# Kernel optimization log

Measured on AMD Instinct MI355X. Metric: run time of the kernel, lower is better.

The kernel has to match this reference:

```python
import jax, jax.numpy as jnp
import numpy as np

N = 100000        # nodes
E = 1600000       # edges
F_IN = 32         # raw node features
C = 128           # out_channels / hidden
L = 5             # gated graph conv layers
G = 1024          # number of graphs in batch


def setup_inputs() -> dict:
    key = jax.random.key(0)
    ks = jax.random.split(key, 12)
    x = jax.random.normal(ks[0], (N, F_IN), dtype=jnp.float32)
    edge_index = jax.random.randint(ks[1], (2, E), 0, N, dtype=jnp.int32)
    edge_weight = jax.random.uniform(ks[2], (E,), dtype=jnp.float32)
    batch = jnp.sort(jax.random.randint(ks[3], (N,), 0, G, dtype=jnp.int32))
    # parameters (scaled small, fan-in style)
    W_emb = jax.random.normal(ks[4], (F_IN, C), dtype=jnp.float32) / np.sqrt(F_IN)
    b_emb = jnp.zeros((C,), dtype=jnp.float32)
    W = jax.random.normal(ks[5], (L, C, C), dtype=jnp.float32) / np.sqrt(C)
    W_ih = jax.random.normal(ks[6], (3 * C, C), dtype=jnp.float32) / np.sqrt(C)
    W_hh = jax.random.normal(ks[7], (3 * C, C), dtype=jnp.float32) / np.sqrt(C)
    b_ih = jnp.zeros((3 * C,), dtype=jnp.float32)
    b_hh = jnp.zeros((3 * C,), dtype=jnp.float32)
    W_prop = jax.random.normal(ks[8], (C, 1), dtype=jnp.float32) / np.sqrt(C)
    b_prop = jnp.zeros((1,), dtype=jnp.float32)
    return {"x": x, "edge_index": edge_index, "edge_weight": edge_weight,
            "batch": batch, "W_emb": W_emb, "b_emb": b_emb, "W": W,
            "W_ih": W_ih, "W_hh": W_hh, "b_ih": b_ih, "b_hh": b_hh,
            "W_prop": W_prop, "b_prop": b_prop}


def _gated_graph_conv(h, src, dst, edge_weight, W, W_ih, W_hh, b_ih, b_hh):
    n_nodes = h.shape[0]

    def step(h, Wl):
        m = h @ Wl                                    # [N,C] per-layer linear
        msg = m[src] * edge_weight[:, None]           # gather + edge weight [E,C]
        agg = jax.ops.segment_sum(msg, dst, num_segments=n_nodes)  # scatter-add
        # torch GRUCell (gate order r, z, n)
        gi = agg @ W_ih.T + b_ih                      # [N,3C]
        gh = h @ W_hh.T + b_hh
        i_r, i_z, i_n = jnp.split(gi, 3, axis=-1)
        h_r, h_z, h_n = jnp.split(gh, 3, axis=-1)
        r = jax.nn.sigmoid(i_r + h_r)
        z = jax.nn.sigmoid(i_z + h_z)
        n = jnp.tanh(i_n + r * h_n)
        h_new = (1.0 - z) * n + z * h
        return h_new, None

    h, _ = jax.lax.scan(step, h, W)
    return h


def reference(x, edge_index, edge_weight, batch, W_emb, b_emb, W,
              W_ih, W_hh, b_ih, b_hh, W_prop, b_prop):
    h0 = x @ W_emb + b_emb                            # node embedding [N,C]
    src, dst = edge_index[0], edge_index[1]
    h = _gated_graph_conv(h0, src, dst, edge_weight, W, W_ih, W_hh, b_ih, b_hh)
    node_prop = h @ W_prop + b_prop                   # [N,1]
    graph_prop = jax.ops.segment_sum(node_prop, batch, num_segments=G)  # [G,1]
    return graph_prop.squeeze(1)                      # [G]
```

## Files before the change

### kernel.cpp

```cpp
#include <hip/hip_runtime.h>

#define NN 100000
#define CC 128
#define EE 1600000
#define GG 1024
#define LL 5

typedef __attribute__((ext_vector_type(8))) short bf16x8;
typedef __attribute__((ext_vector_type(4))) float f32x4;

__device__ __forceinline__ float sigmoidf_(float x) { return 1.0f / (1.0f + __expf(-x)); }
__device__ __forceinline__ float tanhf_(float x) {
  float xx = fminf(15.0f, fmaxf(-15.0f, x));
  float t = __expf(-2.0f * xx);
  return (1.0f - t) / (1.0f + t);
}
__device__ __forceinline__ unsigned short f2bf(float x) {
  unsigned int u = __float_as_uint(x);
  return (unsigned short)((u + 0x7fffu + ((u >> 16) & 1u)) >> 16);
}
__device__ __forceinline__ float bflo(unsigned int u) { return __uint_as_float(u << 16); }
__device__ __forceinline__ float bfhi(unsigned int u) { return __uint_as_float(u & 0xffff0000u); }
__device__ __forceinline__ float bf2f(unsigned short v) { return __uint_as_float((unsigned)v << 16); }

#define PK_WHH 192
#define PK_FUSE (192 * LL)
#define PK_DEG ((NN + 256 + 255) / 256)
#define PK_TOTAL (PK_WHH + PK_FUSE + PK_DEG + 1)

__global__ __launch_bounds__(256) void pack_all_kernel(
    const float* __restrict__ W, const float* __restrict__ W_ih,
    const float* __restrict__ W_hh,
    unsigned short* __restrict__ Whh_p, unsigned short* __restrict__ Wfuse_p,
    int* __restrict__ deg, float* __restrict__ out)
{
  const int b = blockIdx.x;
  const int tid = threadIdx.x;
  if (b < PK_WHH) {
    int t = b * 256 + tid;
    int i = t & 7, l = (t >> 3) & 63, q = t >> 9;
    int ks = q & 3, cb = q >> 2;
    int k = ks * 32 + 8 * (l >> 4) + i;
    int c = cb * 16 + (l & 15);
    Whh_p[t] = f2bf(W_hh[(size_t)c * CC + k]);
  } else if (b < PK_WHH + PK_FUSE) {
    int idx = b - PK_WHH;
    int layer = idx / 192;
    int t = (idx % 192) * 256 + tid;
    int i = t & 7, l = (t >> 3) & 63, q = t >> 9;
    int ks = q & 3, cb = q >> 2;
    int k = ks * 32 + 8 * (l >> 4) + i;
    int c = cb * 16 + (l & 15);
    const float* wl = W + (size_t)layer * CC * CC + (size_t)k * CC;
    const float* wi = W_ih + (size_t)c * CC;
    float acc = 0.f;
    #pragma unroll 8
    for (int j = 0; j < CC; ++j) acc = fmaf(wl[j], wi[j], acc);
    Wfuse_p[(size_t)layer * 49152 + t] = f2bf(acc);
  } else if (b < PK_WHH + PK_FUSE + PK_DEG) {
    int i = (b - PK_WHH - PK_FUSE) * 256 + tid;
    if (i < NN + 256) deg[i] = 0;
  } else {
    #pragma unroll
    for (int i = 0; i < 4; ++i) out[i * 256 + tid] = 0.0f;
  }
}


__global__ __launch_bounds__(256) void hist_kernel(const int* __restrict__ eidx,
                                                   int* __restrict__ deg)
{
  int e = blockIdx.x * blockDim.x + threadIdx.x;
  if (e < EE) atomicAdd(&deg[eidx[EE + e]], 1);
}

__global__ __launch_bounds__(256) void scan1_kernel(const int* __restrict__ deg,
                                                    int* __restrict__ bsum)
{
  __shared__ int red[4];
  int base = blockIdx.x * 1024 + threadIdx.x * 4;
  int s = 0;
  #pragma unroll
  for (int i = 0; i < 4; ++i) { int idx = base + i; if (idx < NN) s += deg[idx]; }
  #pragma unroll
  for (int off = 32; off; off >>= 1) s += __shfl_down(s, off, 64);
  if ((threadIdx.x & 63) == 0) red[threadIdx.x >> 6] = s;
  __syncthreads();
  if (threadIdx.x == 0) bsum[blockIdx.x] = red[0] + red[1] + red[2] + red[3];
}

__global__ __launch_bounds__(64) void scan2_kernel(int* __restrict__ bsum, int nb)
{
  const int lane = threadIdx.x;
  int carry = 0;
  for (int base = 0; base < nb; base += 64) {
    int i = base + lane;
    int v = (i < nb) ? bsum[i] : 0;
    const int orig = v;
    #pragma unroll
    for (int off = 1; off < 64; off <<= 1) {
      int u = __shfl_up(v, off, 64);
      if (lane >= off) v += u;
    }
    if (i < nb) bsum[i] = v - orig + carry;
    carry += __shfl(v, 63, 64);
  }
}

__global__ __launch_bounds__(256) void scan3_kernel(const int* __restrict__ deg,
                                                    const int* __restrict__ bsum,
                                                    int* __restrict__ row_ptr,
                                                    int* __restrict__ cursor)
{
  __shared__ int ts[256];
  const int tid = threadIdx.x;
  const int base = blockIdx.x * 1024 + tid * 4;
  int v[4]; int s = 0;
  #pragma unroll
  for (int i = 0; i < 4; ++i) { int idx = base + i; v[i] = (idx < NN) ? deg[idx] : 0; s += v[i]; }
  ts[tid] = s; __syncthreads();
  for (int off = 1; off < 256; off <<= 1) {
    int t = (tid >= off) ? ts[tid - off] : 0;
    __syncthreads();
    ts[tid] += t;
    __syncthreads();
  }
  int excl = bsum[blockIdx.x] + ts[tid] - s;
  #pragma unroll
  for (int i = 0; i < 4; ++i) {
    int idx = base + i;
    if (idx < NN) { row_ptr[idx] = excl; cursor[idx] = excl; excl += v[i]; }
  }
  if (blockIdx.x == 0 && tid == 0) row_ptr[NN] = EE;
}

__global__ __launch_bounds__(256) void fill_kernel(const int* __restrict__ eidx,
                                                   const float* __restrict__ ew,
                                                   int* __restrict__ cursor,
                                                   int2* __restrict__ csr_sw)
{
  int e = blockIdx.x * blockDim.x + threadIdx.x;
  if (e < EE) {
    int d = eidx[EE + e];
    int p = atomicAdd(&cursor[d], 1);
    csr_sw[p] = make_int2(eidx[e], __float_as_int(ew[e]));
  }
}


__global__ __launch_bounds__(128) void embed_kernel(
    const float* __restrict__ x, const float* __restrict__ W_emb,
    const float* __restrict__ b_emb, unsigned short* __restrict__ h_bf)
{
  const int node = blockIdx.x;
  const int c = threadIdx.x;
  float acc = b_emb[c];
  #pragma unroll
  for (int k = 0; k < 32; ++k)
    acc = fmaf(x[node * 32 + k], W_emb[k * CC + c], acc);
  h_bf[(size_t)node * CC + c] = f2bf(acc);
}

__global__ __launch_bounds__(256) void aggregate_kernel(
    const unsigned short* __restrict__ h_bf, const int* __restrict__ row_ptr,
    const int2* __restrict__ csr_sw, unsigned short* __restrict__ agg_bf)
{
  const int lane = threadIdx.x & 63;
  const int node = (blockIdx.x * blockDim.x + threadIdx.x) >> 6;
  if (node >= NN) return;
  const int q = lane >> 4;
  const int t = lane & 15;
  const int beg = row_ptr[node], end = row_ptr[node + 1];

  float acc[8] = {0.f, 0.f, 0.f, 0.f, 0.f, 0.f, 0.f, 0.f};
  const int last = end - 1;

  for (int j = beg; j < end; j += 16) {
    const int e0 = j + q, e1 = j + 4 + q, e2 = j + 8 + q, e3 = j + 12 + q;
    const int i0 = min(e0, last), i1 = min(e1, last);
    const int i2 = min(e2, last), i3 = min(e3, last);
    const int2 r0 = csr_sw[i0], r1 = csr_sw[i1], r2 = csr_sw[i2], r3 = csr_sw[i3];
    const float w0 = (e0 < end) ? __int_as_float(r0.y) : 0.0f;
    const float w1 = (e1 < end) ? __int_as_float(r1.y) : 0.0f;
    const float w2 = (e2 < end) ? __int_as_float(r2.y) : 0.0f;
    const float w3 = (e3 < end) ? __int_as_float(r3.y) : 0.0f;
    const uint4 u0 = *(const uint4*)(h_bf + (size_t)r0.x * CC + t * 8);
    const uint4 u1 = *(const uint4*)(h_bf + (size_t)r1.x * CC + t * 8);
    const uint4 u2 = *(const uint4*)(h_bf + (size_t)r2.x * CC + t * 8);
    const uint4 u3 = *(const uint4*)(h_bf + (size_t)r3.x * CC + t * 8);
    acc[0] = fmaf(bflo(u0.x), w0, acc[0]); acc[1] = fmaf(bfhi(u0.x), w0, acc[1]);
    acc[2] = fmaf(bflo(u0.y), w0, acc[2]); acc[3] = fmaf(bfhi(u0.y), w0, acc[3]);
    acc[4] = fmaf(bflo(u0.z), w0, acc[4]); acc[5] = fmaf(bfhi(u0.z), w0, acc[5]);
    acc[6] = fmaf(bflo(u0.w), w0, acc[6]); acc[7] = fmaf(bfhi(u0.w), w0, acc[7]);
    acc[0] = fmaf(bflo(u1.x), w1, acc[0]); acc[1] = fmaf(bfhi(u1.x), w1, acc[1]);
    acc[2] = fmaf(bflo(u1.y), w1, acc[2]); acc[3] = fmaf(bfhi(u1.y), w1, acc[3]);
    acc[4] = fmaf(bflo(u1.z), w1, acc[4]); acc[5] = fmaf(bfhi(u1.z), w1, acc[5]);
    acc[6] = fmaf(bflo(u1.w), w1, acc[6]); acc[7] = fmaf(bfhi(u1.w), w1, acc[7]);
    acc[0] = fmaf(bflo(u2.x), w2, acc[0]); acc[1] = fmaf(bfhi(u2.x), w2, acc[1]);
    acc[2] = fmaf(bflo(u2.y), w2, acc[2]); acc[3] = fmaf(bfhi(u2.y), w2, acc[3]);
    acc[4] = fmaf(bflo(u2.z), w2, acc[4]); acc[5] = fmaf(bfhi(u2.z), w2, acc[5]);
    acc[6] = fmaf(bflo(u2.w), w2, acc[6]); acc[7] = fmaf(bfhi(u2.w), w2, acc[7]);
    acc[0] = fmaf(bflo(u3.x), w3, acc[0]); acc[1] = fmaf(bfhi(u3.x), w3, acc[1]);
    acc[2] = fmaf(bflo(u3.y), w3, acc[2]); acc[3] = fmaf(bfhi(u3.y), w3, acc[3]);
    acc[4] = fmaf(bflo(u3.z), w3, acc[4]); acc[5] = fmaf(bfhi(u3.z), w3, acc[5]);
    acc[6] = fmaf(bflo(u3.w), w3, acc[6]); acc[7] = fmaf(bfhi(u3.w), w3, acc[7]);
  }

  #pragma unroll
  for (int i = 0; i < 8; ++i) {
    acc[i] += __shfl_xor(acc[i], 16, 64);
    acc[i] += __shfl_xor(acc[i], 32, 64);
  }

  if (q == 0) {
    uint4 o;
    o.x = (unsigned)f2bf(acc[0]) | ((unsigned)f2bf(acc[1]) << 16);
    o.y = (unsigned)f2bf(acc[2]) | ((unsigned)f2bf(acc[3]) << 16);
    o.z = (unsigned)f2bf(acc[4]) | ((unsigned)f2bf(acc[5]) << 16);
    o.w = (unsigned)f2bf(acc[6]) | ((unsigned)f2bf(acc[7]) << 16);
    *(uint4*)(agg_bf + (size_t)node * CC + t * 8) = o;
  }
}

__global__ __launch_bounds__(256) void gru_kernel(
    const unsigned short* __restrict__ agg_bf, unsigned short* __restrict__ h_bf,
    const unsigned short* __restrict__ Wfuse_p, const unsigned short* __restrict__ Whh_p,
    const float* __restrict__ b_ih, const float* __restrict__ b_hh)
{
  __shared__ unsigned short hbuf[4][32][136];
  const int lane = threadIdx.x & 63;
  const int wave = threadIdx.x >> 6;
  const int node0 = blockIdx.x * 128 + wave * 32;
  if (node0 >= NN) return;
  const int col16 = lane & 15, grp = lane >> 4;

  #pragma unroll
  for (int i = 0; i < 8; ++i) {
    const int chunk = lane + 64 * i;
    const int row = chunk >> 4, c16 = chunk & 15;
    uint4 v = *(const uint4*)(h_bf + (size_t)(node0 + row) * CC + c16 * 8);
    *(uint4*)&hbuf[wave][row][c16 * 8] = v;
  }

  bf16x8 aA[2][4], aH[2][4];
  #pragma unroll
  for (int t = 0; t < 2; ++t) {
    const unsigned short* arow = agg_bf + (size_t)(node0 + t * 16 + col16) * CC + grp * 8;
    #pragma unroll
    for (int ks = 0; ks < 4; ++ks) {
      aA[t][ks] = *(const bf16x8*)(arow + ks * 32);
      aH[t][ks] = *(const bf16x8*)&hbuf[wave][t * 16 + col16][grp * 8 + ks * 32];
    }
  }

  const f32x4 z4 = {0.f, 0.f, 0.f, 0.f};

  #pragma unroll
  for (int cb = 0; cb < 8; ++cb) {
    f32x4 air[2] = {z4, z4}, ahr[2] = {z4, z4};
    f32x4 aiz[2] = {z4, z4}, ahz[2] = {z4, z4};
    f32x4 ain[2] = {z4, z4}, ahn[2] = {z4, z4};
    #pragma unroll
    for (int ks = 0; ks < 4; ++ks) {
      const size_t or_ = (size_t)((cb * 4 + ks) * 64 + lane) * 8;
      const size_t oz_ = (size_t)(((8 + cb) * 4 + ks) * 64 + lane) * 8;
      const size_t on_ = (size_t)(((16 + cb) * 4 + ks) * 64 + lane) * 8;
      bf16x8 bir = *(const bf16x8*)(Wfuse_p + or_);
      bf16x8 bhr = *(const bf16x8*)(Whh_p + or_);
      bf16x8 biz = *(const bf16x8*)(Wfuse_p + oz_);
      bf16x8 bhz = *(const bf16x8*)(Whh_p + oz_);
      bf16x8 bin = *(const bf16x8*)(Wfuse_p + on_);
      bf16x8 bhn = *(const bf16x8*)(Whh_p + on_);
      #pragma unroll
      for (int t = 0; t < 2; ++t) {
        air[t] = __builtin_amdgcn_mfma_f32_16x16x32_bf16(aA[t][ks], bir, air[t], 0, 0, 0);
        ahr[t] = __builtin_amdgcn_mfma_f32_16x16x32_bf16(aH[t][ks], bhr, ahr[t], 0, 0, 0);
        aiz[t] = __builtin_amdgcn_mfma_f32_16x16x32_bf16(aA[t][ks], biz, aiz[t], 0, 0, 0);
        ahz[t] = __builtin_amdgcn_mfma_f32_16x16x32_bf16(aH[t][ks], bhz, ahz[t], 0, 0, 0);
        ain[t] = __builtin_amdgcn_mfma_f32_16x16x32_bf16(aA[t][ks], bin, ain[t], 0, 0, 0);
        ahn[t] = __builtin_amdgcn_mfma_f32_16x16x32_bf16(aH[t][ks], bhn, ahn[t], 0, 0, 0);
      }
    }
    const int o = cb * 16 + col16;
    const float bir_ = b_ih[o],       bhr_ = b_hh[o];
    const float biz_ = b_ih[128 + o], bhz_ = b_hh[128 + o];
    const float bin_ = b_ih[256 + o], bhn_ = b_hh[256 + o];
    #pragma unroll
    for (int t = 0; t < 2; ++t) {
      #pragma unroll
      for (int r = 0; r < 4; ++r) {
        float rr = sigmoidf_(air[t][r] + ahr[t][r] + bir_ + bhr_);
        float zz = sigmoidf_(aiz[t][r] + ahz[t][r] + biz_ + bhz_);
        float nn = tanhf_(ain[t][r] + bin_ + rr * (ahn[t][r] + bhn_));
        const int row = t * 16 + grp * 4 + r;
        float ho = bf2f(hbuf[wave][row][o]);
        h_bf[(size_t)(node0 + row) * CC + o] = f2bf((1.0f - zz) * nn + zz * ho);
      }
    }
  }
}

__global__ __launch_bounds__(256) void prop_kernel(
    const unsigned short* __restrict__ h_bf, const int* __restrict__ batch,
    const float* __restrict__ Wp, const float* __restrict__ bp,
    float* __restrict__ out)
{
  const int lane = threadIdx.x & 63;
  const int wid = (blockIdx.x * blockDim.x + threadIdx.x) >> 6;
  const int nw = (gridDim.x * blockDim.x) >> 6;
  for (int node = wid; node < NN; node += nw) {
    unsigned int u = *(const unsigned int*)(h_bf + (size_t)node * CC + 2 * lane);
    float v = bflo(u) * Wp[2 * lane] + bfhi(u) * Wp[2 * lane + 1];
    #pragma unroll
    for (int off = 32; off > 0; off >>= 1) v += __shfl_down(v, off, 64);
    if (lane == 0) atomicAdd(&out[batch[node]], v + bp[0]);
  }
}

extern "C" void kernel_launch(void* const* d_in, const int* in_sizes, int n_in,
                              void* d_out, int out_size, void* d_ws, size_t ws_size,
                              hipStream_t stream)
{
  const float* x      = (const float*)d_in[0];
  const int*   eidx   = (const int*)d_in[1];
  const float* ew     = (const float*)d_in[2];
  const int*   batch  = (const int*)d_in[3];
  const float* W_emb  = (const float*)d_in[4];
  const float* b_emb  = (const float*)d_in[5];
  const float* W      = (const float*)d_in[6];
  const float* W_ih   = (const float*)d_in[7];
  const float* W_hh   = (const float*)d_in[8];
  const float* b_ih   = (const float*)d_in[9];
  const float* b_hh   = (const float*)d_in[10];
  const float* W_prop = (const float*)d_in[11];
  const float* b_prop = (const float*)d_in[12];
  float* out = (float*)d_out;

  char* p = (char*)d_ws;
  unsigned short* h_bf  = (unsigned short*)p; p += (size_t)NN * CC * sizeof(short);
  unsigned short* agg   = (unsigned short*)p; p += (size_t)NN * CC * sizeof(short);
  int2* csr_sw          = (int2*)p;           p += (size_t)EE * sizeof(int2);
  unsigned short* Wfuse_p = (unsigned short*)p; p += (size_t)LL * 49152 * sizeof(short);
  unsigned short* Whh_p = (unsigned short*)p; p += (size_t)49152 * sizeof(short);
  int* deg     = (int*)p;                     p += (size_t)(NN + 256) * sizeof(int);
  int* row_ptr = (int*)p;                     p += (size_t)(NN + 256) * sizeof(int);
  int* cursor  = (int*)p;                     p += (size_t)(NN + 256) * sizeof(int);
  int* bsum    = (int*)p;                     p += 1024 * sizeof(int);

  const int NB_SCAN = (NN + 1023) / 1024;
  const int EB = (EE + 255) / 256;
  const int MB2 = (NN + 127) / 128;

  pack_all_kernel<<<PK_TOTAL, 256, 0, stream>>>(W, W_ih, W_hh, Whh_p, Wfuse_p, deg, out);

  hist_kernel<<<EB, 256, 0, stream>>>(eidx, deg);
  scan1_kernel<<<NB_SCAN, 256, 0, stream>>>(deg, bsum);
  scan2_kernel<<<1, 64, 0, stream>>>(bsum, NB_SCAN);
  scan3_kernel<<<NB_SCAN, 256, 0, stream>>>(deg, bsum, row_ptr, cursor);
  fill_kernel<<<EB, 256, 0, stream>>>(eidx, ew, cursor, csr_sw);

  embed_kernel<<<NN, 128, 0, stream>>>(x, W_emb, b_emb, h_bf);

  for (int l = 0; l < LL; ++l) {
    aggregate_kernel<<<(NN + 3) / 4, 256, 0, stream>>>(h_bf, row_ptr, csr_sw, agg);
    gru_kernel<<<MB2, 256, 0, stream>>>(agg, h_bf,
                                        Wfuse_p + (size_t)l * 49152, Whh_p, b_ih, b_hh);
  }

  prop_kernel<<<2048, 256, 0, stream>>>(h_bf, batch, W_prop, b_prop, out);
}
```

Before: 881.4 us.

## Switch GRU matmuls to 32x32x16 MFMA and deepen aggregate edge unroll

The GRU kernel moves from 16x16x32 bf16 MFMA tiles (two row tiles, eight column blocks) to 32x32x16 MFMA tiles (one 32-row tile, four column blocks), and the packed weight layouts are changed to match. This is meant to halve the number of B-fragment weight loads per wave and use the larger MFMA shape. Separately, the aggregate kernel processes 32 edges per iteration instead of 16, issuing all index and feature loads before the FMAs so more gathers are in flight. The costs are higher register pressure from the 16-wide accumulators and the extra in-flight loads, and a non-unrolled outer loop in the GRU kernel.

```diff
diff --git a/kernel.cpp b/kernel.cpp
--- a/kernel.cpp
+++ b/kernel.cpp
@@ -7,7 +7,7 @@
 #define LL 5
 
 typedef __attribute__((ext_vector_type(8))) short bf16x8;
-typedef __attribute__((ext_vector_type(4))) float f32x4;
+typedef __attribute__((ext_vector_type(16))) float f32x16;
 
 __device__ __forceinline__ float sigmoidf_(float x) { return 1.0f / (1.0f + __expf(-x)); }
 __device__ __forceinline__ float tanhf_(float x) {
@@ -39,20 +39,20 @@
   if (b < PK_WHH) {
     int t = b * 256 + tid;
     int i = t & 7, l = (t >> 3) & 63, q = t >> 9;
-    int ks = q & 3, cb = q >> 2;
-    int k = ks * 32 + 8 * (l >> 4) + i;
-    int c = cb * 16 + (l & 15);
-    Whh_p[t] = f2bf(W_hh[(size_t)c * CC + k]);
+    int ks = q & 7, cb = q >> 3;
+    int k = ks * 16 + 8 * (l >> 5) + i;
+    int o = cb * 32 + (l & 31);
+    Whh_p[t] = f2bf(W_hh[(size_t)o * CC + k]);
   } else if (b < PK_WHH + PK_FUSE) {
     int idx = b - PK_WHH;
     int layer = idx / 192;
     int t = (idx % 192) * 256 + tid;
     int i = t & 7, l = (t >> 3) & 63, q = t >> 9;
-    int ks = q & 3, cb = q >> 2;
-    int k = ks * 32 + 8 * (l >> 4) + i;
-    int c = cb * 16 + (l & 15);
+    int ks = q & 7, cb = q >> 3;
+    int k = ks * 16 + 8 * (l >> 5) + i;
+    int o = cb * 32 + (l & 31);
     const float* wl = W + (size_t)layer * CC * CC + (size_t)k * CC;
-    const float* wi = W_ih + (size_t)c * CC;
+    const float* wi = W_ih + (size_t)o * CC;
     float acc = 0.f;
     #pragma unroll 8
     for (int j = 0; j < CC; ++j) acc = fmaf(wl[j], wi[j], acc);
@@ -175,19 +175,30 @@
   float acc[8] = {0.f, 0.f, 0.f, 0.f, 0.f, 0.f, 0.f, 0.f};
   const int last = end - 1;
 
-  for (int j = beg; j < end; j += 16) {
-    const int e0 = j + q, e1 = j + 4 + q, e2 = j + 8 + q, e3 = j + 12 + q;
-    const int i0 = min(e0, last), i1 = min(e1, last);
-    const int i2 = min(e2, last), i3 = min(e3, last);
-    const int2 r0 = csr_sw[i0], r1 = csr_sw[i1], r2 = csr_sw[i2], r3 = csr_sw[i3];
+  for (int j = beg; j < end; j += 32) {
+    const int e0 = j + q,      e1 = j + 4 + q,  e2 = j + 8 + q,  e3 = j + 12 + q;
+    const int e4 = j + 16 + q, e5 = j + 20 + q, e6 = j + 24 + q, e7 = j + 28 + q;
+    const int2 r0 = csr_sw[min(e0, last)], r1 = csr_sw[min(e1, last)];
+    const int2 r2 = csr_sw[min(e2, last)], r3 = csr_sw[min(e3, last)];
+    const int2 r4 = csr_sw[min(e4, last)], r5 = csr_sw[min(e5, last)];
+    const int2 r6 = csr_sw[min(e6, last)], r7 = csr_sw[min(e7, last)];
+    const uint4 u0 = *(const uint4*)(h_bf + (size_t)r0.x * CC + t * 8);
+    const uint4 u1 = *(const uint4*)(h_bf + (size_t)r1.x * CC + t * 8);
+    const uint4 u2 = *(const uint4*)(h_bf + (size_t)r2.x * CC + t * 8);
+    const uint4 u3 = *(const uint4*)(h_bf + (size_t)r3.x * CC + t * 8);
+    const uint4 u4 = *(const uint4*)(h_bf + (size_t)r4.x * CC + t * 8);
+    const uint4 u5 = *(const uint4*)(h_bf + (size_t)r5.x * CC + t * 8);
+    const uint4 u6 = *(const uint4*)(h_bf + (size_t)r6.x * CC + t * 8);
+    const uint4 u7 = *(const uint4*)(h_bf + (size_t)r7.x * CC + t * 8);
     const float w0 = (e0 < end) ? __int_as_float(r0.y) : 0.0f;
     const float w1 = (e1 < end) ? __int_as_float(r1.y) : 0.0f;
     const float w2 = (e2 < end) ? __int_as_float(r2.y) : 0.0f;
     const float w3 = (e3 < end) ? __int_as_float(r3.y) : 0.0f;
-    const uint4 u0 = *(const uint4*)(h_bf + (size_t)r0.x * CC + t * 8);
-    const uint4 u1 = *(const uint4*)(h_bf + (size_t)r1.x * CC + t * 8);
-    const uint4 u2 = *(const uint4*)(h_bf + (size_t)r2.x * CC + t * 8);
-    const uint4 u3 = *(const uint4*)(h_bf + (size_t)r3.x * CC + t * 8);
+    const float w4 = (e4 < end) ? __int_as_float(r4.y) : 0.0f;
+    const float w5 = (e5 < end) ? __int_as_float(r5.y) : 0.0f;
+    const float w6 = (e6 < end) ? __int_as_float(r6.y) : 0.0f;
+    const float w7 = (e7 < end) ? __int_as_float(r7.y) : 0.0f;
+
     acc[0] = fmaf(bflo(u0.x), w0, acc[0]); acc[1] = fmaf(bfhi(u0.x), w0, acc[1]);
     acc[2] = fmaf(bflo(u0.y), w0, acc[2]); acc[3] = fmaf(bfhi(u0.y), w0, acc[3]);
     acc[4] = fmaf(bflo(u0.z), w0, acc[4]); acc[5] = fmaf(bfhi(u0.z), w0, acc[5]);
@@ -204,6 +215,22 @@
     acc[2] = fmaf(bflo(u3.y), w3, acc[2]); acc[3] = fmaf(bfhi(u3.y), w3, acc[3]);
     acc[4] = fmaf(bflo(u3.z), w3, acc[4]); acc[5] = fmaf(bfhi(u3.z), w3, acc[5]);
     acc[6] = fmaf(bflo(u3.w), w3, acc[6]); acc[7] = fmaf(bfhi(u3.w), w3, acc[7]);
+    acc[0] = fmaf(bflo(u4.x), w4, acc[0]); acc[1] = fmaf(bfhi(u4.x), w4, acc[1]);
+    acc[2] = fmaf(bflo(u4.y), w4, acc[2]); acc[3] = fmaf(bfhi(u4.y), w4, acc[3]);
+    acc[4] = fmaf(bflo(u4.z), w4, acc[4]); acc[5] = fmaf(bfhi(u4.z), w4, acc[5]);
+    acc[6] = fmaf(bflo(u4.w), w4, acc[6]); acc[7] = fmaf(bfhi(u4.w), w4, acc[7]);
+    acc[0] = fmaf(bflo(u5.x), w5, acc[0]); acc[1] = fmaf(bfhi(u5.x), w5, acc[1]);
+    acc[2] = fmaf(bflo(u5.y), w5, acc[2]); acc[3] = fmaf(bfhi(u5.y), w5, acc[3]);
+    acc[4] = fmaf(bflo(u5.z), w5, acc[4]); acc[5] = fmaf(bfhi(u5.z), w5, acc[5]);
+    acc[6] = fmaf(bflo(u5.w), w5, acc[6]); acc[7] = fmaf(bfhi(u5.w), w5, acc[7]);
+    acc[0] = fmaf(bflo(u6.x), w6, acc[0]); acc[1] = fmaf(bfhi(u6.x), w6, acc[1]);
+    acc[2] = fmaf(bflo(u6.y), w6, acc[2]); acc[3] = fmaf(bfhi(u6.y), w6, acc[3]);
+    acc[4] = fmaf(bflo(u6.z), w6, acc[4]); acc[5] = fmaf(bfhi(u6.z), w6, acc[5]);
+    acc[6] = fmaf(bflo(u6.w), w6, acc[6]); acc[7] = fmaf(bfhi(u6.w), w6, acc[7]);
+    acc[0] = fmaf(bflo(u7.x), w7, acc[0]); acc[1] = fmaf(bfhi(u7.x), w7, acc[1]);
+    acc[2] = fmaf(bflo(u7.y), w7, acc[2]); acc[3] = fmaf(bfhi(u7.y), w7, acc[3]);
+    acc[4] = fmaf(bflo(u7.z), w7, acc[4]); acc[5] = fmaf(bfhi(u7.z), w7, acc[5]);
+    acc[6] = fmaf(bflo(u7.w), w7, acc[6]); acc[7] = fmaf(bfhi(u7.w), w7, acc[7]);
   }
 
   #pragma unroll
@@ -232,7 +259,8 @@
   const int wave = threadIdx.x >> 6;
   const int node0 = blockIdx.x * 128 + wave * 32;
   if (node0 >= NN) return;
-  const int col16 = lane & 15, grp = lane >> 4;
+  const int l31 = lane & 31;
+  const int kg = lane >> 5;
 
   #pragma unroll
   for (int i = 0; i < 8; ++i) {
@@ -242,60 +270,50 @@
     *(uint4*)&hbuf[wave][row][c16 * 8] = v;
   }
 
-  bf16x8 aA[2][4], aH[2][4];
-  #pragma unroll
-  for (int t = 0; t < 2; ++t) {
-    const unsigned short* arow = agg_bf + (size_t)(node0 + t * 16 + col16) * CC + grp * 8;
-    #pragma unroll
-    for (int ks = 0; ks < 4; ++ks) {
-      aA[t][ks] = *(const bf16x8*)(arow + ks * 32);
-      aH[t][ks] = *(const bf16x8*)&hbuf[wave][t * 16 + col16][grp * 8 + ks * 32];
+  bf16x8 aA[8], aH[8];
+  {
+    const unsigned short* arow = agg_bf + (size_t)(node0 + l31) * CC + kg * 8;
+    #pragma unroll
+    for (int ks = 0; ks < 8; ++ks) {
+      aA[ks] = *(const bf16x8*)(arow + ks * 16);
+      aH[ks] = *(const bf16x8*)&hbuf[wave][l31][ks * 16 + kg * 8];
     }
   }
 
-  const f32x4 z4 = {0.f, 0.f, 0.f, 0.f};
-
-  #pragma unroll
-  for (int cb = 0; cb < 8; ++cb) {
-    f32x4 air[2] = {z4, z4}, ahr[2] = {z4, z4};
-    f32x4 aiz[2] = {z4, z4}, ahz[2] = {z4, z4};
-    f32x4 ain[2] = {z4, z4}, ahn[2] = {z4, z4};
-    #pragma unroll
-    for (int ks = 0; ks < 4; ++ks) {
-      const size_t or_ = (size_t)((cb * 4 + ks) * 64 + lane) * 8;
-      const size_t oz_ = (size_t)(((8 + cb) * 4 + ks) * 64 + lane) * 8;
-      const size_t on_ = (size_t)(((16 + cb) * 4 + ks) * 64 + lane) * 8;
-      bf16x8 bir = *(const bf16x8*)(Wfuse_p + or_);
-      bf16x8 bhr = *(const bf16x8*)(Whh_p + or_);
-      bf16x8 biz = *(const bf16x8*)(Wfuse_p + oz_);
-      bf16x8 bhz = *(const bf16x8*)(Whh_p + oz_);
-      bf16x8 bin = *(const bf16x8*)(Wfuse_p + on_);
-      bf16x8 bhn = *(const bf16x8*)(Whh_p + on_);
-      #pragma unroll
-      for (int t = 0; t < 2; ++t) {
-        air[t] = __builtin_amdgcn_mfma_f32_16x16x32_bf16(aA[t][ks], bir, air[t], 0, 0, 0);
-        ahr[t] = __builtin_amdgcn_mfma_f32_16x16x32_bf16(aH[t][ks], bhr, ahr[t], 0, 0, 0);
-        aiz[t] = __builtin_amdgcn_mfma_f32_16x16x32_bf16(aA[t][ks], biz, aiz[t], 0, 0, 0);
-        ahz[t] = __builtin_amdgcn_mfma_f32_16x16x32_bf16(aH[t][ks], bhz, ahz[t], 0, 0, 0);
-        ain[t] = __builtin_amdgcn_mfma_f32_16x16x32_bf16(aA[t][ks], bin, ain[t], 0, 0, 0);
-        ahn[t] = __builtin_amdgcn_mfma_f32_16x16x32_bf16(aH[t][ks], bhn, ahn[t], 0, 0, 0);
-      }
+  const f32x16 z16 = {0.f};
+
+  for (int cc = 0; cc < 4; ++cc) {
+    f32x16 air = z16, ahr = z16, aiz = z16, ahz = z16, ain = z16, ahn = z16;
+    #pragma unroll
+    for (int ks = 0; ks < 8; ++ks) {
+      const size_t fr = (size_t)(((cc     ) * 8 + ks) * 64 + lane) * 8;
+      const size_t fz = (size_t)(((4 + cc) * 8 + ks) * 64 + lane) * 8;
+      const size_t fn = (size_t)(((8 + cc) * 8 + ks) * 64 + lane) * 8;
+      bf16x8 bir = *(const bf16x8*)(Wfuse_p + fr);
+      bf16x8 bhr = *(const bf16x8*)(Whh_p + fr);
+      bf16x8 biz = *(const bf16x8*)(Wfuse_p + fz);
+      bf16x8 bhz = *(const bf16x8*)(Whh_p + fz);
+      bf16x8 bin = *(const bf16x8*)(Wfuse_p + fn);
+      bf16x8 bhn = *(const bf16x8*)(Whh_p + fn);
+      air = __builtin_amdgcn_mfma_f32_32x32x16_bf16(aA[ks], bir, air, 0, 0, 0);
+      ahr = __builtin_amdgcn_mfma_f32_32x32x16_bf16(aH[ks], bhr, ahr, 0, 0, 0);
+      aiz = __builtin_amdgcn_mfma_f32_32x32x16_bf16(aA[ks], biz, aiz, 0, 0, 0);
+      ahz = __builtin_amdgcn_mfma_f32_32x32x16_bf16(aH[ks], bhz, ahz, 0, 0, 0);
+      ain = __builtin_amdgcn_mfma_f32_32x32x16_bf16(aA[ks], bin, ain, 0, 0, 0);
+      ahn = __builtin_amdgcn_mfma_f32_32x32x16_bf16(aH[ks], bhn, ahn, 0, 0, 0);
     }
-    const int o = cb * 16 + col16;
+    const int o = cc * 32 + l31;
     const float bir_ = b_ih[o],       bhr_ = b_hh[o];
     const float biz_ = b_ih[128 + o], bhz_ = b_hh[128 + o];
     const float bin_ = b_ih[256 + o], bhn_ = b_hh[256 + o];
     #pragma unroll
-    for (int t = 0; t < 2; ++t) {
-      #pragma unroll
-      for (int r = 0; r < 4; ++r) {
-        float rr = sigmoidf_(air[t][r] + ahr[t][r] + bir_ + bhr_);
-        float zz = sigmoidf_(aiz[t][r] + ahz[t][r] + biz_ + bhz_);
-        float nn = tanhf_(ain[t][r] + bin_ + rr * (ahn[t][r] + bhn_));
-        const int row = t * 16 + grp * 4 + r;
-        float ho = bf2f(hbuf[wave][row][o]);
-        h_bf[(size_t)(node0 + row) * CC + o] = f2bf((1.0f - zz) * nn + zz * ho);
-      }
+    for (int r = 0; r < 16; ++r) {
+      const int row = (r & 3) + 8 * (r >> 2) + 4 * kg;
+      float rr = sigmoidf_(air[r] + ahr[r] + bir_ + bhr_);
+      float zz = sigmoidf_(aiz[r] + ahz[r] + biz_ + bhz_);
+      float nn = tanhf_(ain[r] + bin_ + rr * (ahn[r] + bhn_));
+      float ho = bf2f(hbuf[wave][row][o]);
+      h_bf[(size_t)(node0 + row) * CC + o] = f2bf((1.0f - zz) * nn + zz * ho);
     }
   }
 }
```

Result: slower. 1.337 ms (+51.7%).
